# Kernel optimization log

Hardware: AMD Instinct MI355X
Metric: run time of the kernel (lower is better)

The kernel has to match this reference:

```python
import jax, jax.numpy as jnp
import numpy as np

B, C, H, W = 8, 512, 64, 64
WS, NH = 8, 16
HD = C // NH
SCALE = float(HD) ** -0.5
L = WS * WS  # tokens per window
BN_EPS = 1e-5


def _rel_index():
    # Swin relative position index, (L, L) int table into (2*WS-1)^2 bias rows
    ch = np.arange(WS)
    coords = np.stack(np.meshgrid(ch, ch, indexing='ij'))  # (2, WS, WS)
    cf = coords.reshape(2, -1)
    rel = cf[:, :, None] - cf[:, None, :]
    rel = rel.transpose(1, 2, 0).copy()
    rel[:, :, 0] += WS - 1
    rel[:, :, 1] += WS - 1
    rel[:, :, 0] *= 2 * WS - 1
    return jnp.asarray(rel.sum(-1))

REL_IDX = _rel_index()


def conv2d(x, w, pad=0, groups=1):
    return jax.lax.conv_general_dilated(
        x, w, (1, 1), [(pad, pad), (pad, pad)],
        feature_group_count=groups,
        dimension_numbers=('NCHW', 'OIHW', 'NCHW'))


def bn(x, g, b):
    # eval-mode BatchNorm with running_mean=0, running_var=1 (fresh init)
    inv = 1.0 / np.sqrt(1.0 + BN_EPS)
    return g[None, :, None, None] * (x * inv) + b[None, :, None, None]


def avgpool(x, kh, kw, ph, pw):
    # torch AvgPool2d: zero padding, count_include_pad=True
    s = jax.lax.reduce_window(x, 0.0, jax.lax.add, (1, 1, kh, kw), (1, 1, 1, 1),
                              ((0, 0), (0, 0), (ph, ph), (pw, pw)))
    return s / (kh * kw)


def setup_inputs() -> dict:
    key = jax.random.key(0)
    ks = jax.random.split(key, 8)
    r = lambda k, s: jax.random.normal(k, s, dtype=jnp.float32) * 0.02
    return {
        'x': jax.random.normal(ks[0], (B, C, H, W), dtype=jnp.float32),
        'w_lc1': r(ks[1], (C, C, 1, 1)),
        'g1': jnp.ones((C,), jnp.float32), 'b1': jnp.zeros((C,), jnp.float32),
        'w_lc2': r(ks[2], (C, C, 3, 3)),
        'g2': jnp.ones((C,), jnp.float32), 'b2': jnp.zeros((C,), jnp.float32),
        'w_qkv': r(ks[3], (3 * C, C, 1, 1)),
        'rel_table': r(ks[4], ((2 * WS - 1) * (2 * WS - 1), NH)),
        'w_dw': r(ks[5], (C, 1, WS, WS)),
        'g3': jnp.ones((C,), jnp.float32), 'b3': jnp.zeros((C,), jnp.float32),
        'w_pw': r(ks[6], (C, C, 1, 1)),
    }


def reference(x, w_lc1, g1, b1, w_lc2, g2, b2, w_qkv, rel_table, w_dw, g3, b3, w_pw):
    # local branch: 1x1 conv+BN  +  3x3 conv+BN
    local = bn(conv2d(x, w_lc1), g1, b1) + bn(conv2d(x, w_lc2, pad=1), g2, b2)

    # H, W divisible by WS -> pad() is a no-op; Hp, Wp = H, W
    hh, ww = H // WS, W // WS
    qkv = conv2d(x, w_qkv)  # (B, 3C, H, W)
    # 'b (qkv h d) (hh ws1) (ww ws2) -> qkv (b hh ww) h (ws1 ws2) d'
    qkv = qkv.reshape(B, 3, NH, HD, hh, WS, ww, WS)
    qkv = qkv.transpose(1, 0, 4, 6, 2, 5, 7, 3).reshape(3, B * hh * ww, NH, L, HD)
    q, k, v = qkv[0], qkv[1], qkv[2]

    dots = jnp.einsum('bhid,bhjd->bhij', q, k) * SCALE  # (Bw, NH, L, L)
    bias = rel_table[REL_IDX]                            # (L, L, NH)
    dots = dots + bias.transpose(2, 0, 1)[None]
    attn = jax.nn.softmax(dots, axis=-1)
    out = jnp.einsum('bhij,bhjd->bhid', attn, v)         # (Bw, NH, L, HD)

    # '(b hh ww) h (ws1 ws2) d -> b (h d) (hh ws1) (ww ws2)'
    out = out.reshape(B, hh, ww, NH, WS, WS, HD)
    out = out.transpose(0, 3, 6, 1, 4, 2, 5).reshape(B, C, H, W)

    ax = avgpool(jnp.pad(out, ((0, 0), (0, 0), (0, 1), (0, 0)), mode='reflect'),
                 WS, 1, WS // 2 - 1, 0)
    ay = avgpool(jnp.pad(out, ((0, 0), (0, 0), (0, 0), (0, 1)), mode='reflect'),
                 1, WS, 0, WS // 2 - 1)
    out = ax + ay + local

    # pad_out + SeparableConvBN(kernel=WS): depthwise conv -> BN -> 1x1 conv
    out = jnp.pad(out, ((0, 0), (0, 0), (0, 1), (0, 1)), mode='reflect')
    out = conv2d(out, w_dw, pad=(WS - 1) // 2, groups=C)
    out = bn(out, g3, b3)
    out = conv2d(out, w_pw)
    return out[:, :, :H, :W]
```

## Files before the change

### kernel.cpp

```cpp
#include <hip/hip_runtime.h>

#define INVBN 0.9999950000374997f
#define ATT_SCALE 0.17677669529663687f

typedef short bf16x8 __attribute__((ext_vector_type(8)));
typedef float f32x4  __attribute__((ext_vector_type(4)));
typedef unsigned short us8v __attribute__((ext_vector_type(8)));

#define AS1C(p) ((const __attribute__((address_space(1))) void*)(p))
#define AS3(p)  ((__attribute__((address_space(3))) void*)(p))

__device__ __forceinline__ float bf2f(unsigned short u) {
    return __uint_as_float(((unsigned)u) << 16);
}
__device__ __forceinline__ unsigned short f2bf(float f) {
    unsigned u = __float_as_uint(f);
    u += 0x7FFFu + ((u >> 16) & 1u);
    return (unsigned short)(u >> 16);
}

__global__ __launch_bounds__(256)
void repack_kernel(const float* __restrict__ W2, const float* __restrict__ W1,
                   const float* __restrict__ Wq, const float* __restrict__ Wp,
                   const float* __restrict__ g1, const float* __restrict__ g2,
                   const float* __restrict__ b1, const float* __restrict__ b2,
                   unsigned short* __restrict__ Wt, unsigned short* __restrict__ WqO,
                   unsigned short* __restrict__ WpO, float* __restrict__ bsum)
{
    int i = blockIdx.x * 256 + threadIdx.x;
    if (i < 512) bsum[i] = b1[i] + b2[i];
    if (i < 786432) WqO[i] = f2bf(Wq[i]);
    if (i < 262144) WpO[i] = f2bf(Wp[i]);
    if (i >= 2359296) return;
    int tap = i / 262144;
    int rem = i - tap * 262144;
    int m   = rem >> 9;
    float v = g2[m] * INVBN * W2[(size_t)rem * 9 + tap];
    if (tap == 4) v = fmaf(g1[m] * INVBN, W1[rem], v);
    Wt[i] = f2bf(v);
}

__global__ __launch_bounds__(256)
void bias_precompute_kernel(const float* __restrict__ RT, float* __restrict__ biasM)
{
    int idx = blockIdx.x * 256 + threadIdx.x;
    int h = idx >> 10, rem = idx & 1023;
    int frag = rem >> 6, lane = rem & 63;
    int fi = frag >> 2, fj = frag & 3;
    int q  = 16 * fj + (lane & 15);
    int kb = 16 * fi + ((lane >> 4) << 2);
    int yi = q >> 3, xi = q & 7;
    float4 o;
    float* op = (float*)&o;
#pragma unroll
    for (int r = 0; r < 4; ++r) {
        int j = kb + r;
        int ridx = (yi - (j >> 3) + 7) * 15 + (xi - (j & 7) + 7);
        op[r] = RT[ridx * 16 + h];
    }
    *(float4*)&biasM[(size_t)idx * 4] = o;
}

__global__ __launch_bounds__(256)
void pad_transpose_kernel(const float* __restrict__ X, unsigned short* __restrict__ XT)
{
    int ph = blockIdx.x;
    int b  = blockIdx.y;
    int t  = threadIdx.x;
    unsigned short* rowbase = XT + ((size_t)b * 4356 + (size_t)ph * 66) * 512;
    uint4 z = make_uint4(0, 0, 0, 0);
    if (ph == 0 || ph == 65) {
        uint4* p4 = (uint4*)rowbase;
        for (int i = t; i < 4224; i += 256) p4[i] = z;
        return;
    }
    if (t < 64)       ((uint4*)rowbase)[t] = z;
    else if (t < 128) ((uint4*)(rowbase + 65 * 512))[t - 64] = z;

    int h = ph - 1;
    __shared__ float tile[64][65];
    const float* xb = X + (size_t)b * 512 * 4096 + h * 64;
    for (int cc = 0; cc < 8; ++cc) {
        int c0 = cc * 64;
        __syncthreads();
#pragma unroll
        for (int i = 0; i < 4; ++i) {
            int cl = i * 16 + (t >> 4);
            int w0 = (t & 15) * 4;
            *(float4*)&tile[cl][w0] =
                *(const float4*)&xb[(size_t)(c0 + cl) * 4096 + w0];
        }
        __syncthreads();
#pragma unroll
        for (int it = 0; it < 2; ++it) {
            int wl = it * 32 + (t >> 3);
            int cs = (t & 7) * 8;
            us8v v;
#pragma unroll
            for (int e = 0; e < 8; ++e) v[e] = f2bf(tile[cs + e][wl]);
            *(us8v*)&rowbase[(size_t)(1 + wl) * 512 + c0 + cs] = v;
        }
    }
}

template<int NTAPS>
__global__ __launch_bounds__(256, 2)
void mfma_gemm256(const unsigned short* __restrict__ A,
                  const unsigned short* __restrict__ Bw,
                  const float* __restrict__ bias,
                  unsigned short* __restrict__ Out, int M, int MB)
{
    __shared__ __align__(16) unsigned short ldsbuf[24576];

    const int t    = threadIdx.x;
    const int wid  = t >> 6, lane = t & 63;
    const int wr   = wid >> 1, wc = wid & 1;
    const int lrow = lane & 15, lk = lane >> 4;

    const int nwg = gridDim.x;
    const int id  = blockIdx.x;
    const int cid = (id & 7) * (nwg >> 3) + (id >> 3);
    const int by  = cid % MB;
    const int rst = cid / MB;
    const int bx  = rst & 15;
    const int bz  = rst >> 4;

    const int n0 = bx * 256;
    const int m0 = by * 128;
    const unsigned short* Ab = A + (size_t)bz * (4356 * 512);
    unsigned short* Ob = Out + (size_t)bz * ((size_t)M * 4096);

    const int rsub = t >> 2, ch = t & 3;
    const int chs  = ch ^ ((rsub >> 1) & 3);
    const unsigned short* asrc[4];
    const unsigned short* bsrc[2];
#pragma unroll
    for (int i = 0; i < 4; ++i) {
        int p = n0 + i * 64 + rsub;
        int h = p >> 6, w = p & 63;
        asrc[i] = Ab + (size_t)((h + 1) * 66 + (w + 1)) * 512 + chs * 8;
    }
#pragma unroll
    for (int j = 0; j < 2; ++j)
        bsrc[j] = Bw + (size_t)(m0 + j * 64 + rsub) * 512 + chs * 8;

    f32x4 acc[8][4] = {};
    const int ck0 = (lk ^ ((lrow >> 1) & 3)) * 8;

    auto aScal = [&](int tt) -> int {
        if (NTAPS == 1) return tt * 32;
        int tap = tt >> 4;
        return (tap / 3 - 1) * (66 * 512) + (tap % 3 - 1) * 512 + (tt & 15) * 32;
    };
    auto bScal = [&](int tt) -> int {
        if (NTAPS == 1) return tt * 32;
        return (tt >> 4) * (M * 512) + (tt & 15) * 32;
    };
    auto STAGE = [&](int parity, int tt) {
        unsigned short* dst = ldsbuf + parity * 12288;
        int ao = aScal(tt), bo = bScal(tt);
#pragma unroll
        for (int i = 0; i < 4; ++i)
            __builtin_amdgcn_global_load_lds(
                AS1C(asrc[i] + ao), AS3(dst + (i * 64 + rsub) * 32 + ch * 8), 16, 0, 0);
#pragma unroll
        for (int j = 0; j < 2; ++j)
            __builtin_amdgcn_global_load_lds(
                AS1C(bsrc[j] + bo), AS3(dst + 8192 + (j * 64 + rsub) * 32 + ch * 8), 16, 0, 0);
    };
    auto COMPUTE = [&](int parity) {
        const unsigned short* Ak = ldsbuf + parity * 12288;
        const unsigned short* Bk = Ak + 8192;
        bf16x8 af[8], bf[4];
#pragma unroll
        for (int f = 0; f < 8; ++f)
            af[f] = *(const bf16x8*)&Ak[(wr * 128 + f * 16 + lrow) * 32 + ck0];
#pragma unroll
        for (int g = 0; g < 4; ++g)
            bf[g] = *(const bf16x8*)&Bk[(wc * 64 + g * 16 + lrow) * 32 + ck0];
        __builtin_amdgcn_s_setprio(1);
#pragma unroll
        for (int f = 0; f < 8; ++f)
#pragma unroll
            for (int g = 0; g < 4; ++g)
                acc[f][g] = __builtin_amdgcn_mfma_f32_16x16x32_bf16(
                    af[f], bf[g], acc[f][g], 0, 0, 0);
        __builtin_amdgcn_s_setprio(0);
    };

    constexpr int NT = NTAPS * 16;

    STAGE(0, 0);
#pragma unroll 2
    for (int tt = 0; tt < NT; ++tt) {
        if (tt + 1 < NT) {
            STAGE((tt + 1) & 1, tt + 1);
            asm volatile("s_waitcnt vmcnt(6)" ::: "memory");
        } else {
            asm volatile("s_waitcnt vmcnt(0)" ::: "memory");
        }
        __builtin_amdgcn_s_barrier();
        COMPUTE(tt & 1);
        __builtin_amdgcn_s_barrier();
    }

#pragma unroll
    for (int g = 0; g < 4; ++g) {
        int m = m0 + wc * 64 + g * 16 + lrow;
        float bv = bias ? bias[m] : 0.f;
        size_t mrow = (size_t)m * 4096;
#pragma unroll
        for (int f = 0; f < 8; ++f) {
            int nb = n0 + wr * 128 + f * 16 + lk * 4;
            f32x4 a4 = acc[f][g];
            ushort4 o;
            o.x = f2bf(a4[0] + bv);
            o.y = f2bf(a4[1] + bv);
            o.z = f2bf(a4[2] + bv);
            o.w = f2bf(a4[3] + bv);
            *(ushort4*)&Ob[mrow + nb] = o;
        }
    }
}

__global__ __launch_bounds__(256)
void mfma_gemm_f32out(const unsigned short* __restrict__ A,
                      const unsigned short* __restrict__ Bw,
                      float* __restrict__ Out, int M)
{
    __shared__ short As[128 * 64];
    __shared__ short Bs[128 * 64];

    const int t  = threadIdx.x;
    const int n0 = blockIdx.x * 128;
    const int m0 = blockIdx.y * 128;
    const int b  = blockIdx.z;
    const unsigned short* Ab = A + (size_t)b * (4096 * 512);
    float* Ob = Out + (size_t)b * ((size_t)M * 4096);

    const int trow = t >> 3;
    const int csrc = (t & 7) ^ (trow & 7);
    const unsigned short* aSrc[4];
    const unsigned short* bSrc[4];
#pragma unroll
    for (int i = 0; i < 4; ++i) {
        int r = i * 32 + trow;
        aSrc[i] = Ab + ((size_t)(n0 + r) * 512 + csrc * 8);
        bSrc[i] = Bw + ((size_t)(m0 + r) * 512 + csrc * 8);
    }
    short* aDst = As + (t & 192) * 8;
    short* bDst = Bs + (t & 192) * 8;

    const int lane = t & 63;
    const int wv = t >> 6, wr = wv >> 1, wc = wv & 1;
    const int lrow = lane & 15, lk = lane >> 4;
    int aOff[4][2], bOff[4][2];
#pragma unroll
    for (int f = 0; f < 4; ++f)
#pragma unroll
        for (int kk = 0; kk < 2; ++kk) {
            int ra = wr * 64 + f * 16 + lrow;
            aOff[f][kk] = ra * 64 + ((kk * 4 + lk) ^ (ra & 7)) * 8;
            int rb = wc * 64 + f * 16 + lrow;
            bOff[f][kk] = rb * 64 + ((kk * 4 + lk) ^ (rb & 7)) * 8;
        }

    f32x4 acc[4][4] = {};

#pragma unroll 1
    for (int ks = 0; ks < 8; ++ks) {
        const int k0 = ks * 64;
        __syncthreads();
#pragma unroll
        for (int i = 0; i < 4; ++i) {
            __builtin_amdgcn_global_load_lds(
                AS1C(aSrc[i] + k0), AS3(aDst + i * 2048), 16, 0, 0);
            __builtin_amdgcn_global_load_lds(
                AS1C(bSrc[i] + k0), AS3(bDst + i * 2048), 16, 0, 0);
        }
        __syncthreads();
        bf16x8 av[4][2], bv[4][2];
#pragma unroll
        for (int f = 0; f < 4; ++f) {
            av[f][0] = *(const bf16x8*)&As[aOff[f][0]];
            av[f][1] = *(const bf16x8*)&As[aOff[f][1]];
            bv[f][0] = *(const bf16x8*)&Bs[bOff[f][0]];
            bv[f][1] = *(const bf16x8*)&Bs[bOff[f][1]];
        }
#pragma unroll
        for (int kk = 0; kk < 2; ++kk)
#pragma unroll
            for (int fn = 0; fn < 4; ++fn)
#pragma unroll
                for (int fm = 0; fm < 4; ++fm)
                    acc[fn][fm] = __builtin_amdgcn_mfma_f32_16x16x32_bf16(
                        av[fn][kk], bv[fm][kk], acc[fn][fm], 0, 0, 0);
    }

#pragma unroll
    for (int fm = 0; fm < 4; ++fm) {
        int m = m0 + wc * 64 + fm * 16 + lrow;
        size_t mrow = (size_t)m * 4096;
#pragma unroll
        for (int fn = 0; fn < 4; ++fn) {
            int nb = n0 + wr * 64 + fn * 16 + lk * 4;
            f32x4 a4 = acc[fn][fm];
            *(float4*)&Ob[mrow + nb] = make_float4(a4[0], a4[1], a4[2], a4[3]);
        }
    }
}

__global__ __launch_bounds__(256)
void attn_mfma_kernel(const unsigned short* __restrict__ QKV,
                      const float* __restrict__ biasM,
                      unsigned short* __restrict__ OutB)
{
    __shared__ short smem[4 * 9216];
    int t = threadIdx.x;
    int wv = t >> 6, lane = t & 63;
    int wing = blockIdx.x >> 2;
    int head = (blockIdx.x & 3) * 4 + wv;
    int b    = blockIdx.y;
    int hhi = wing >> 3, wwi = wing & 7;
    int sp0 = hhi * 512 + wwi * 8;
    int ch0 = head * 32;
    const unsigned short* Qg = QKV + (size_t)b * 1536 * 4096;

    short* Qtm = smem + wv * 9216;
    short* Ktm = Qtm + 2304;
    short* Pq  = Qtm + 4608;

    {
        int d  = lane & 31;
        int rb = lane >> 5;
#pragma unroll
        for (int i = 0; i < 4; ++i) {
            int r = rb + 2 * i;
            us8v q8 = *(const us8v*)&Qg[(size_t)(ch0 + d) * 4096 + sp0 + r * 64];
            us8v k8 = *(const us8v*)&Qg[(size_t)(512 + ch0 + d) * 4096 + sp0 + r * 64];
#pragma unroll
            for (int e = 0; e < 8; ++e) {
                Qtm[(r * 8 + e) * 36 + d] = (short)q8[e];
                Ktm[(r * 8 + e) * 36 + d] = (short)k8[e];
            }
        }
    }

    int lrow = lane & 15, lk = lane >> 4;

    bf16x8 kf[4], qf[4];
#pragma unroll
    for (int f = 0; f < 4; ++f) {
        kf[f] = *(const bf16x8*)&Ktm[(lrow + 16 * f) * 36 + lk * 8];
        qf[f] = *(const bf16x8*)&Qtm[(lrow + 16 * f) * 36 + lk * 8];
    }
    f32x4 s[4][4] = {};
#pragma unroll
    for (int fi = 0; fi < 4; ++fi)
#pragma unroll
        for (int fj = 0; fj < 4; ++fj)
            s[fi][fj] = __builtin_amdgcn_mfma_f32_16x16x32_bf16(
                kf[fi], qf[fj], s[fi][fj], 0, 0, 0);

    const float* bM = biasM + (size_t)head * 4096;
    float rs[4];
#pragma unroll
    for (int fj = 0; fj < 4; ++fj) {
        float v[4][4];
#pragma unroll
        for (int fi = 0; fi < 4; ++fi) {
            float4 bv = *(const float4*)&bM[((fi * 4 + fj) * 64 + lane) * 4];
            const float* bvp = (const float*)&bv;
#pragma unroll
            for (int r = 0; r < 4; ++r)
                v[fi][r] = fmaf(s[fi][fj][r], ATT_SCALE, bvp[r]);
        }
        float m = -1e30f;
#pragma unroll
        for (int fi = 0; fi < 4; ++fi)
#pragma unroll
            for (int r = 0; r < 4; ++r) m = fmaxf(m, v[fi][r]);
        m = fmaxf(m, __shfl_xor(m, 16));
        m = fmaxf(m, __shfl_xor(m, 32));
        float ev[4][4];
        float sum = 0.f;
#pragma unroll
        for (int fi = 0; fi < 4; ++fi)
#pragma unroll
            for (int r = 0; r < 4; ++r) {
                ev[fi][r] = __expf(v[fi][r] - m);
                sum += ev[fi][r];
            }
        sum += __shfl_xor(sum, 16);
        sum += __shfl_xor(sum, 32);
        rs[fj] = 1.f / sum;
#pragma unroll
        for (int fi = 0; fi < 4; ++fi) {
            unsigned p0 = (unsigned)f2bf(ev[fi][0]) | ((unsigned)f2bf(ev[fi][1]) << 16);
            unsigned p1 = (unsigned)f2bf(ev[fi][2]) | ((unsigned)f2bf(ev[fi][3]) << 16);
            *(uint2*)&Pq[(lrow + 16 * fj) * 72 + 16 * fi + lk * 4] = make_uint2(p0, p1);
        }
    }

    f32x4 o[2][4] = {};
#pragma unroll
    for (int ks = 0; ks < 2; ++ks) {
        bf16x8 vf[2], pf[4];
#pragma unroll
        for (int fid = 0; fid < 2; ++fid)
            vf[fid] = *(const bf16x8*)&Qg[(size_t)(1024 + ch0 + 16 * fid + lrow) * 4096
                                          + sp0 + (lk + 4 * ks) * 64];
#pragma unroll
        for (int fjq = 0; fjq < 4; ++fjq)
            pf[fjq] = *(const bf16x8*)&Pq[(lrow + 16 * fjq) * 72 + ks * 32 + lk * 8];
#pragma unroll
        for (int fid = 0; fid < 2; ++fid)
#pragma unroll
            for (int fjq = 0; fjq < 4; ++fjq)
                o[fid][fjq] = __builtin_amdgcn_mfma_f32_16x16x32_bf16(
                    vf[fid], pf[fjq], o[fid][fjq], 0, 0, 0);
    }

    unsigned short* Out = OutB + (size_t)b * 512 * 4096;
#pragma unroll
    for (int fjq = 0; fjq < 4; ++fjq) {
        int q  = lrow + 16 * fjq;
        int sp = sp0 + ((q >> 3) << 6) + (q & 7);
        float rr = rs[fjq];
#pragma unroll
        for (int fid = 0; fid < 2; ++fid)
#pragma unroll
            for (int r = 0; r < 4; ++r) {
                int dch = 16 * fid + lk * 4 + r;
                Out[(size_t)(ch0 + dch) * 4096 + sp] = f2bf(o[fid][fjq][r] * rr);
            }
    }
}

__global__ __launch_bounds__(256)
void pooldw_kernel(const unsigned short* __restrict__ A, const unsigned short* __restrict__ L,
                   const float* __restrict__ Wd,
                   const float* __restrict__ g3, const float* __restrict__ b3,
                   unsigned short* __restrict__ U)
{
    int bc = blockIdx.x;
    int c  = bc & 511;
    __shared__ float pad[72][72];
    int t = threadIdx.x;
    float* pf = &pad[0][0];
#pragma unroll
    for (int i = 0; i < 21; ++i) {
        int e = i * 256 + t;
        if (e < 5184) pf[e] = 0.f;
    }
    __syncthreads();

    const unsigned short* ap = A + (size_t)bc * 4096;
#pragma unroll
    for (int i = 0; i < 4; ++i) {
        int idx = i * 256 + t;
        int y = idx >> 4, x4 = (idx & 15) * 4;
        ushort4 a4 = ((const ushort4*)ap)[idx];
        *(float4*)&pad[3 + y][4 + x4] =
            make_float4(bf2f(a4.x), bf2f(a4.y), bf2f(a4.z), bf2f(a4.w));
    }
    if (t < 64)       pad[67][4 + t] = bf2f(ap[62 * 64 + t]);
    else if (t < 128) { int y = t - 64; pad[3 + y][68] = bf2f(ap[y * 64 + 62]); }
    else if (t == 128) pad[67][68] = bf2f(ap[62 * 64 + 62]);
    __syncthreads();

    const unsigned short* lp = L + (size_t)bc * 4096;
    int u  = t & 15, rr = t >> 4;
    int w0 = u * 4;
    float4 res[4];
#pragma unroll
    for (int g = 0; g < 4; ++g) {
        int h = g * 16 + rr;
        float4 sx = make_float4(0.f, 0.f, 0.f, 0.f);
#pragma unroll
        for (int i = 0; i < 8; ++i) {
            float4 v = *(const float4*)&pad[h + i][4 + w0];
            sx.x += v.x; sx.y += v.y; sx.z += v.z; sx.w += v.w;
        }
        float win[12];
        *(float4*)&win[0] = *(const float4*)&pad[3 + h][w0];
        *(float4*)&win[4] = *(const float4*)&pad[3 + h][w0 + 4];
        *(float4*)&win[8] = *(const float4*)&pad[3 + h][w0 + 8];
        float4 sy = make_float4(0.f, 0.f, 0.f, 0.f);
#pragma unroll
        for (int i = 0; i < 8; ++i) {
            sy.x += win[1 + i];
            sy.y += win[2 + i];
            sy.z += win[3 + i];
            sy.w += win[4 + i];
        }
        ushort4 l4 = *(const ushort4*)&lp[h * 64 + w0];
        res[g].x = fmaf(0.125f, sx.x + sy.x, bf2f(l4.x));
        res[g].y = fmaf(0.125f, sx.y + sy.y, bf2f(l4.y));
        res[g].z = fmaf(0.125f, sx.z + sy.z, bf2f(l4.z));
        res[g].w = fmaf(0.125f, sx.w + sy.w, bf2f(l4.w));
    }
    __syncthreads();

#pragma unroll
    for (int g = 0; g < 4; ++g) {
        int h = g * 16 + rr;
        *(float4*)&pad[3 + h][4 + w0] = res[g];
    }
    __syncthreads();
    if (t < 64)       pad[67][4 + t] = pad[65][4 + t];
    else if (t < 128) { int y = t - 64; pad[3 + y][68] = pad[3 + y][66]; }
    else if (t == 128) pad[67][68] = pad[65][66];
    __syncthreads();

    const float* wdp = Wd + c * 64;
    float gc  = g3[c] * INVBN;
    float bcv = b3[c];
#pragma unroll
    for (int g = 0; g < 4; ++g) {
        int h = g * 16 + rr;
        float a0 = 0.f, a1 = 0.f, a2 = 0.f, a3 = 0.f;
#pragma unroll
        for (int i = 0; i < 8; ++i) {
            float win[12];
            *(float4*)&win[0] = *(const float4*)&pad[h + i][w0];
            *(float4*)&win[4] = *(const float4*)&pad[h + i][w0 + 4];
            *(float4*)&win[8] = *(const float4*)&pad[h + i][w0 + 8];
#pragma unroll
            for (int j = 0; j < 8; ++j) {
                float wv = wdp[i * 8 + j];
                a0 = fmaf(wv, win[1 + j], a0);
                a1 = fmaf(wv, win[2 + j], a1);
                a2 = fmaf(wv, win[3 + j], a2);
                a3 = fmaf(wv, win[4 + j], a3);
            }
        }
        ushort4 o;
        o.x = f2bf(gc * a0 + bcv);
        o.y = f2bf(gc * a1 + bcv);
        o.z = f2bf(gc * a2 + bcv);
        o.w = f2bf(gc * a3 + bcv);
        *(ushort4*)&U[(size_t)bc * 4096 + h * 64 + w0] = o;
    }
}

__global__ __launch_bounds__(256)
void transpose_cp_kernel(const unsigned short* __restrict__ U, unsigned short* __restrict__ Ut)
{
    int pt = blockIdx.x;
    int b  = blockIdx.y;
    const unsigned short* Ub = U + (size_t)b * 512 * 4096;
    unsigned short* Utb = Ut + (size_t)b * 4096 * 512;
    __shared__ unsigned short tile[64][72];
    int t = threadIdx.x;
    int p0 = pt * 64;

    for (int cc = 0; cc < 8; ++cc) {
        int c0 = cc * 64;
        __syncthreads();
        {
            int cl = t >> 2, px = (t & 3) * 16;
            const unsigned short* src = &Ub[(size_t)(c0 + cl) * 4096 + p0 + px];
            *(us8v*)&tile[cl][px]     = *(const us8v*)src;
            *(us8v*)&tile[cl][px + 8] = *(const us8v*)(src + 8);
        }
        __syncthreads();
        {
            int pl = t >> 2, cx = (t & 3) * 16;
            us8v o0, o1;
#pragma unroll
            for (int e = 0; e < 8; ++e) {
                o0[e] = tile[cx + e][pl];
                o1[e] = tile[cx + 8 + e][pl];
            }
            unsigned short* dst = &Utb[(size_t)(p0 + pl) * 512 + c0 + cx];
            *(us8v*)dst       = o0;
            *(us8v*)(dst + 8) = o1;
        }
    }
}

extern "C" void kernel_launch(void* const* d_in, const int* in_sizes, int n_in,
                              void* d_out, int out_size, void* d_ws, size_t ws_size,
                              hipStream_t stream)
{
    (void)in_sizes; (void)n_in; (void)out_size;
    const float* x     = (const float*)d_in[0];
    const float* w_lc1 = (const float*)d_in[1];
    const float* g1    = (const float*)d_in[2];
    const float* b1    = (const float*)d_in[3];
    const float* w_lc2 = (const float*)d_in[4];
    const float* g2    = (const float*)d_in[5];
    const float* b2    = (const float*)d_in[6];
    const float* w_qkv = (const float*)d_in[7];
    const float* rt    = (const float*)d_in[8];
    const float* w_dw  = (const float*)d_in[9];
    const float* g3    = (const float*)d_in[10];
    const float* b3    = (const float*)d_in[11];
    const float* w_pw  = (const float*)d_in[12];
    float* out = (float*)d_out;

    unsigned short* S        = (unsigned short*)d_ws;
    unsigned short* local_us = S;
    unsigned short* xt_us    = S + 16777216;
    unsigned short* attnO    = xt_us;
    unsigned short* u_us     = xt_us;
    unsigned short* wt3_us   = S + 34619392;
    unsigned short* wq_us    = S + 36978688;
    unsigned short* wpw_us   = S + 37765120;
    float*          bsum     = (float*)(S + 38027264);
    float*          biasM    = (float*)(S + 38028288);
    unsigned short* qkv_us   = S + 38552576;
    unsigned short* ut_us    = local_us;

    const bool full = ws_size >= (size_t)(38552576 + 50331648) * 2;

    repack_kernel<<<dim3(9216), 256, 0, stream>>>(w_lc2, w_lc1, w_qkv, w_pw,
                                                  g1, g2, b1, b2,
                                                  wt3_us, wq_us, wpw_us, bsum);
    bias_precompute_kernel<<<dim3(64), 256, 0, stream>>>(rt, biasM);
    pad_transpose_kernel<<<dim3(66, 8), 256, 0, stream>>>(x, xt_us);
    mfma_gemm256<9><<<dim3(512), 256, 0, stream>>>(
        xt_us, wt3_us, bsum, local_us, 512, 4);

    if (full) {
        mfma_gemm256<1><<<dim3(1536), 256, 0, stream>>>(
            xt_us, wq_us, nullptr, qkv_us, 1536, 12);
        attn_mfma_kernel<<<dim3(256, 8), 256, 0, stream>>>(qkv_us, biasM, attnO);
    } else {
        for (int b = 0; b < 8; ++b) {
            mfma_gemm256<1><<<dim3(192), 256, 0, stream>>>(
                xt_us + (size_t)b * 4356 * 512, wq_us, nullptr, qkv_us, 1536, 12);
            attn_mfma_kernel<<<dim3(256, 1), 256, 0, stream>>>(
                qkv_us, biasM, attnO + (size_t)b * 2097152);
        }
    }

    pooldw_kernel<<<dim3(4096), 256, 0, stream>>>(attnO, local_us, w_dw, g3, b3, u_us);
    transpose_cp_kernel<<<dim3(64, 8), 256, 0, stream>>>(u_us, ut_us);
    mfma_gemm_f32out<<<dim3(32, 4, 8), 256, 0, stream>>>(
        ut_us, wpw_us, out, 512);
}
```

Measured before the change: 481.2 us.

## Triple-buffer GEMM staging, coalesce attention stores, widen pool/dwconv tiles, fuse bias precompute

The MFMA GEMM moves from double to triple LDS buffering, so each tile is prefetched two iterations ahead and global-load latency is better hidden. This raises LDS use per block, which may affect occupancy at two blocks per CU. The attention kernel's output is staged through LDS so channel rows are written as 16-byte vectors instead of scattered 2-byte stores. The pooling/depthwise kernel computes 8 outputs per thread instead of 4 for more register reuse, and the relative-bias precompute is folded into the repack kernel to save a launch.

```diff
diff --git a/kernel.cpp b/kernel.cpp
--- a/kernel.cpp
+++ b/kernel.cpp
@@ -24,13 +24,32 @@
                    const float* __restrict__ Wq, const float* __restrict__ Wp,
                    const float* __restrict__ g1, const float* __restrict__ g2,
                    const float* __restrict__ b1, const float* __restrict__ b2,
+                   const float* __restrict__ RT,
                    unsigned short* __restrict__ Wt, unsigned short* __restrict__ WqO,
-                   unsigned short* __restrict__ WpO, float* __restrict__ bsum)
+                   unsigned short* __restrict__ WpO, float* __restrict__ bsum,
+                   float* __restrict__ biasM)
 {
     int i = blockIdx.x * 256 + threadIdx.x;
     if (i < 512) bsum[i] = b1[i] + b2[i];
     if (i < 786432) WqO[i] = f2bf(Wq[i]);
     if (i < 262144) WpO[i] = f2bf(Wp[i]);
+    if (i < 16384) {
+        int h = i >> 10, rem = i & 1023;
+        int frag = rem >> 6, lane = rem & 63;
+        int fi = frag >> 2, fj = frag & 3;
+        int q  = 16 * fj + (lane & 15);
+        int kb = 16 * fi + ((lane >> 4) << 2);
+        int yi = q >> 3, xi = q & 7;
+        float4 o;
+        float* op = (float*)&o;
+#pragma unroll
+        for (int r = 0; r < 4; ++r) {
+            int j = kb + r;
+            int ridx = (yi - (j >> 3) + 7) * 15 + (xi - (j & 7) + 7);
+            op[r] = RT[ridx * 16 + h];
+        }
+        *(float4*)&biasM[(size_t)i * 4] = o;
+    }
     if (i >= 2359296) return;
     int tap = i / 262144;
     int rem = i - tap * 262144;
@@ -38,27 +57,6 @@
     float v = g2[m] * INVBN * W2[(size_t)rem * 9 + tap];
     if (tap == 4) v = fmaf(g1[m] * INVBN, W1[rem], v);
     Wt[i] = f2bf(v);
-}
-
-__global__ __launch_bounds__(256)
-void bias_precompute_kernel(const float* __restrict__ RT, float* __restrict__ biasM)
-{
-    int idx = blockIdx.x * 256 + threadIdx.x;
-    int h = idx >> 10, rem = idx & 1023;
-    int frag = rem >> 6, lane = rem & 63;
-    int fi = frag >> 2, fj = frag & 3;
-    int q  = 16 * fj + (lane & 15);
-    int kb = 16 * fi + ((lane >> 4) << 2);
-    int yi = q >> 3, xi = q & 7;
-    float4 o;
-    float* op = (float*)&o;
-#pragma unroll
-    for (int r = 0; r < 4; ++r) {
-        int j = kb + r;
-        int ridx = (yi - (j >> 3) + 7) * 15 + (xi - (j & 7) + 7);
-        op[r] = RT[ridx * 16 + h];
-    }
-    *(float4*)&biasM[(size_t)idx * 4] = o;
 }
 
 __global__ __launch_bounds__(256)
@@ -110,7 +108,7 @@
                   const float* __restrict__ bias,
                   unsigned short* __restrict__ Out, int M, int MB)
 {
-    __shared__ __align__(16) unsigned short ldsbuf[24576];
+    __shared__ __align__(16) unsigned short ldsbuf[36864];
 
     const int t    = threadIdx.x;
     const int wid  = t >> 6, lane = t & 63;
@@ -156,8 +154,8 @@
         if (NTAPS == 1) return tt * 32;
         return (tt >> 4) * (M * 512) + (tt & 15) * 32;
     };
-    auto STAGE = [&](int parity, int tt) {
-        unsigned short* dst = ldsbuf + parity * 12288;
+    auto STAGE = [&](int bufk, int tt) {
+        unsigned short* dst = ldsbuf + bufk * 12288;
         int ao = aScal(tt), bo = bScal(tt);
 #pragma unroll
         for (int i = 0; i < 4; ++i)
@@ -168,8 +166,8 @@
             __builtin_amdgcn_global_load_lds(
                 AS1C(bsrc[j] + bo), AS3(dst + 8192 + (j * 64 + rsub) * 32 + ch * 8), 16, 0, 0);
     };
-    auto COMPUTE = [&](int parity) {
-        const unsigned short* Ak = ldsbuf + parity * 12288;
+    auto COMPUTE = [&](int bufk) {
+        const unsigned short* Ak = ldsbuf + bufk * 12288;
         const unsigned short* Bk = Ak + 8192;
         bf16x8 af[8], bf[4];
 #pragma unroll
@@ -191,17 +189,22 @@
     constexpr int NT = NTAPS * 16;
 
     STAGE(0, 0);
-#pragma unroll 2
+    STAGE(1, 1);
+    int cur = 0, nxt = 1, prv = 2;
+#pragma unroll 1
     for (int tt = 0; tt < NT; ++tt) {
-        if (tt + 1 < NT) {
-            STAGE((tt + 1) & 1, tt + 1);
+        if (tt + 2 < NT) {
+            STAGE(prv, tt + 2);
+            asm volatile("s_waitcnt vmcnt(6)" ::: "memory");
+        } else if (tt + 1 < NT) {
             asm volatile("s_waitcnt vmcnt(6)" ::: "memory");
         } else {
             asm volatile("s_waitcnt vmcnt(0)" ::: "memory");
         }
         __builtin_amdgcn_s_barrier();
-        COMPUTE(tt & 1);
+        COMPUTE(cur);
         __builtin_amdgcn_s_barrier();
+        int tmp = prv; prv = cur; cur = nxt; nxt = tmp;
     }
 
 #pragma unroll
@@ -421,19 +424,25 @@
                     vf[fid], pf[fjq], o[fid][fjq], 0, 0, 0);
     }
 
+#pragma unroll
+    for (int fjq = 0; fjq < 4; ++fjq) {
+        int q = lrow + 16 * fjq;
+        float rr = rs[fjq];
+#pragma unroll
+        for (int fid = 0; fid < 2; ++fid) {
+            int dch = 16 * fid + lk * 4;
+#pragma unroll
+            for (int r = 0; r < 4; ++r)
+                Pq[(dch + r) * 72 + q] = (short)f2bf(o[fid][fjq][r] * rr);
+        }
+    }
     unsigned short* Out = OutB + (size_t)b * 512 * 4096;
 #pragma unroll
-    for (int fjq = 0; fjq < 4; ++fjq) {
-        int q  = lrow + 16 * fjq;
-        int sp = sp0 + ((q >> 3) << 6) + (q & 7);
-        float rr = rs[fjq];
-#pragma unroll
-        for (int fid = 0; fid < 2; ++fid)
-#pragma unroll
-            for (int r = 0; r < 4; ++r) {
-                int dch = 16 * fid + lk * 4 + r;
-                Out[(size_t)(ch0 + dch) * 4096 + sp] = f2bf(o[fid][fjq][r] * rr);
-            }
+    for (int j = 0; j < 4; ++j) {
+        int dch  = lane & 31;
+        int tokc = (lane >> 5) + 2 * j;
+        us8v vv = *(const us8v*)&Pq[dch * 72 + tokc * 8];
+        *(us8v*)&Out[(size_t)(ch0 + dch) * 4096 + sp0 + tokc * 64] = vv;
     }
 }
 
@@ -470,42 +479,43 @@
     __syncthreads();
 
     const unsigned short* lp = L + (size_t)bc * 4096;
-    int u  = t & 15, rr = t >> 4;
-    int w0 = u * 4;
-    float4 res[4];
-#pragma unroll
-    for (int g = 0; g < 4; ++g) {
-        int h = g * 16 + rr;
-        float4 sx = make_float4(0.f, 0.f, 0.f, 0.f);
+    int u  = t & 7, rr = t >> 3;
+    int w0 = u * 8;
+    float res[2][8];
+#pragma unroll
+    for (int g = 0; g < 2; ++g) {
+        int h = g * 32 + rr;
+        float4 sxlo = make_float4(0.f, 0.f, 0.f, 0.f);
+        float4 sxhi = make_float4(0.f, 0.f, 0.f, 0.f);
 #pragma unroll
         for (int i = 0; i < 8; ++i) {
-            float4 v = *(const float4*)&pad[h + i][4 + w0];
-            sx.x += v.x; sx.y += v.y; sx.z += v.z; sx.w += v.w;
-        }
-        float win[12];
-        *(float4*)&win[0] = *(const float4*)&pad[3 + h][w0];
-        *(float4*)&win[4] = *(const float4*)&pad[3 + h][w0 + 4];
-        *(float4*)&win[8] = *(const float4*)&pad[3 + h][w0 + 8];
-        float4 sy = make_float4(0.f, 0.f, 0.f, 0.f);
-#pragma unroll
-        for (int i = 0; i < 8; ++i) {
-            sy.x += win[1 + i];
-            sy.y += win[2 + i];
-            sy.z += win[3 + i];
-            sy.w += win[4 + i];
-        }
-        ushort4 l4 = *(const ushort4*)&lp[h * 64 + w0];
-        res[g].x = fmaf(0.125f, sx.x + sy.x, bf2f(l4.x));
-        res[g].y = fmaf(0.125f, sx.y + sy.y, bf2f(l4.y));
-        res[g].z = fmaf(0.125f, sx.z + sy.z, bf2f(l4.z));
-        res[g].w = fmaf(0.125f, sx.w + sy.w, bf2f(l4.w));
+            float4 a = *(const float4*)&pad[h + i][4 + w0];
+            float4 bq = *(const float4*)&pad[h + i][8 + w0];
+            sxlo.x += a.x; sxlo.y += a.y; sxlo.z += a.z; sxlo.w += a.w;
+            sxhi.x += bq.x; sxhi.y += bq.y; sxhi.z += bq.z; sxhi.w += bq.w;
+        }
+        float sx[8] = {sxlo.x, sxlo.y, sxlo.z, sxlo.w, sxhi.x, sxhi.y, sxhi.z, sxhi.w};
+        float win[16];
+        *(float4*)&win[0]  = *(const float4*)&pad[3 + h][w0];
+        *(float4*)&win[4]  = *(const float4*)&pad[3 + h][w0 + 4];
+        *(float4*)&win[8]  = *(const float4*)&pad[3 + h][w0 + 8];
+        *(float4*)&win[12] = *(const float4*)&pad[3 + h][w0 + 12];
+        us8v l8 = *(const us8v*)&lp[h * 64 + w0];
+#pragma unroll
+        for (int p = 0; p < 8; ++p) {
+            float sy = 0.f;
+#pragma unroll
+            for (int i = 1; i <= 8; ++i) sy += win[p + i];
+            res[g][p] = fmaf(0.125f, sx[p] + sy, bf2f((unsigned short)l8[p]));
+        }
     }
     __syncthreads();
 
 #pragma unroll
-    for (int g = 0; g < 4; ++g) {
-        int h = g * 16 + rr;
-        *(float4*)&pad[3 + h][4 + w0] = res[g];
+    for (int g = 0; g < 2; ++g) {
+        int h = g * 32 + rr;
+        *(float4*)&pad[3 + h][4 + w0] = make_float4(res[g][0], res[g][1], res[g][2], res[g][3]);
+        *(float4*)&pad[3 + h][8 + w0] = make_float4(res[g][4], res[g][5], res[g][6], res[g][7]);
     }
     __syncthreads();
     if (t < 64)       pad[67][4 + t] = pad[65][4 + t];
@@ -517,30 +527,30 @@
     float gc  = g3[c] * INVBN;
     float bcv = b3[c];
 #pragma unroll
-    for (int g = 0; g < 4; ++g) {
-        int h = g * 16 + rr;
-        float a0 = 0.f, a1 = 0.f, a2 = 0.f, a3 = 0.f;
+    for (int g = 0; g < 2; ++g) {
+        int h = g * 32 + rr;
+        float acc2[8];
+#pragma unroll
+        for (int p = 0; p < 8; ++p) acc2[p] = 0.f;
 #pragma unroll
         for (int i = 0; i < 8; ++i) {
-            float win[12];
-            *(float4*)&win[0] = *(const float4*)&pad[h + i][w0];
-            *(float4*)&win[4] = *(const float4*)&pad[h + i][w0 + 4];
-            *(float4*)&win[8] = *(const float4*)&pad[h + i][w0 + 8];
+            float win[16];
+            *(float4*)&win[0]  = *(const float4*)&pad[h + i][w0];
+            *(float4*)&win[4]  = *(const float4*)&pad[h + i][w0 + 4];
+            *(float4*)&win[8]  = *(const float4*)&pad[h + i][w0 + 8];
+            *(float4*)&win[12] = *(const float4*)&pad[h + i][w0 + 12];
 #pragma unroll
             for (int j = 0; j < 8; ++j) {
                 float wv = wdp[i * 8 + j];
-                a0 = fmaf(wv, win[1 + j], a0);
-                a1 = fmaf(wv, win[2 + j], a1);
-                a2 = fmaf(wv, win[3 + j], a2);
-                a3 = fmaf(wv, win[4 + j], a3);
+#pragma unroll
+                for (int p = 0; p < 8; ++p)
+                    acc2[p] = fmaf(wv, win[p + 1 + j], acc2[p]);
             }
         }
-        ushort4 o;
-        o.x = f2bf(gc * a0 + bcv);
-        o.y = f2bf(gc * a1 + bcv);
-        o.z = f2bf(gc * a2 + bcv);
-        o.w = f2bf(gc * a3 + bcv);
-        *(ushort4*)&U[(size_t)bc * 4096 + h * 64 + w0] = o;
+        us8v o8;
+#pragma unroll
+        for (int p = 0; p < 8; ++p) o8[p] = (short)f2bf(gc * acc2[p] + bcv);
+        *(us8v*)&U[(size_t)bc * 4096 + h * 64 + w0] = o8;
     }
 }
 
@@ -616,9 +626,8 @@
     const bool full = ws_size >= (size_t)(38552576 + 50331648) * 2;
 
     repack_kernel<<<dim3(9216), 256, 0, stream>>>(w_lc2, w_lc1, w_qkv, w_pw,
-                                                  g1, g2, b1, b2,
-                                                  wt3_us, wq_us, wpw_us, bsum);
-    bias_precompute_kernel<<<dim3(64), 256, 0, stream>>>(rt, biasM);
+                                                  g1, g2, b1, b2, rt,
+                                                  wt3_us, wq_us, wpw_us, bsum, biasM);
     pad_transpose_kernel<<<dim3(66, 8), 256, 0, stream>>>(x, xt_us);
     mfma_gemm256<9><<<dim3(512), 256, 0, stream>>>(
         xt_us, wt3_us, bsum, local_us, 512, 4);
```

After: 481.1 us. Within noise of the previous version (-0.0%).
